# Kernel tuning notes

Hardware: AMD Instinct MI355X
Metric: run time of the kernel (lower is better)

## Reference

```python
import jax, jax.numpy as jnp
import numpy as np

B, S, D = 1, 2048, 1024
H = 16            # num_heads
DH = D // H       # head dim = 64
WIN = 128         # local window size
DIL = 4           # dilation rate


def setup_inputs() -> dict:
    key = jax.random.key(0)
    k1, k2, k3 = jax.random.split(key, 3)
    x = jax.random.normal(k1, (B, S, D), jnp.float32)
    w_qkv = jax.random.normal(k2, (D, 3 * D), jnp.float32) * 0.02
    w_out = jax.random.normal(k3, (D, D), jnp.float32) * 0.02
    return {"x": x, "w_qkv": w_qkv, "w_out": w_out}


def reference(x, w_qkv, w_out):
    b, s, d = x.shape
    scale = 1.0 / np.sqrt(DH).astype(np.float32)

    qkv = x @ w_qkv                                   # [B,S,3D]
    q, k, v = jnp.split(qkv, 3, axis=-1)
    q = q.reshape(b, s, H, DH)
    k = k.reshape(b, s, H, DH)
    v = v.reshape(b, s, H, DH)

    # ---- local window attention: attend within non-overlapping windows ----
    nw = s // WIN
    qw = q.reshape(b, nw, WIN, H, DH)
    kw = k.reshape(b, nw, WIN, H, DH)
    vw = v.reshape(b, nw, WIN, H, DH)
    s_loc = jnp.einsum('bnihd,bnjhd->bnhij', qw, kw) * scale
    p_loc = jax.nn.softmax(s_loc, axis=-1)
    o_loc = jnp.einsum('bnhij,bnjhd->bnihd', p_loc, vw).reshape(b, s, H, DH)

    # ---- dilated attention: attend within each stride-DIL residue class ----
    n = s // DIL
    # seq index = i*DIL + g  -> position i within dilation group g
    qd = q.reshape(b, n, DIL, H, DH)
    kd = k.reshape(b, n, DIL, H, DH)
    vd = v.reshape(b, n, DIL, H, DH)
    s_dil = jnp.einsum('bighd,bjghd->bghij', qd, kd) * scale
    p_dil = jax.nn.softmax(s_dil, axis=-1)
    o_dil = jnp.einsum('bghij,bjghd->bighd', p_dil, vd).reshape(b, s, H, DH)

    # ---- global full attention ----
    s_glb = jnp.einsum('bihd,bjhd->bhij', q, k) * scale
    p_glb = jax.nn.softmax(s_glb, axis=-1)
    o_glb = jnp.einsum('bhij,bjhd->bihd', p_glb, v)

    # fuse the three scales (uniform average) and project out
    o = (o_loc + o_dil + o_glb) * (1.0 / 3.0)
    return o.reshape(b, s, d) @ w_out
```

## Files before the change

kernel.cpp:

```cpp
#include <hip/hip_runtime.h>
#include <hip/hip_bf16.h>


typedef __attribute__((ext_vector_type(8))) short s8v;
typedef __attribute__((ext_vector_type(4))) float f4v;

#define QSCALE 0.18033688011112042f

__device__ __forceinline__ short f2bf(float f) {
  union { float f; unsigned u; } x; x.f = f;
  unsigned r = (x.u + 0x7FFF + ((x.u >> 16) & 1)) >> 16;
  return (short)r;
}
__device__ __forceinline__ f4v mfma16(s8v a, s8v b, f4v c) {
  return __builtin_amdgcn_mfma_f32_16x16x32_bf16(a, b, c, 0, 0, 0);
}
__device__ __forceinline__ void load_lds16(const void* g, void* l) {
  __builtin_amdgcn_global_load_lds(
      (const __attribute__((address_space(1))) unsigned int*)g,
      (__attribute__((address_space(3))) unsigned int*)l, 16, 0, 0);
}
__device__ __forceinline__ float exp2f_fast(float x) {
  return __builtin_amdgcn_exp2f(x);
}

__global__ __launch_bounds__(256)
void fill_const_kernel(float* __restrict__ out, int n, float v) {
  int i = blockIdx.x * 256 + threadIdx.x;
  if (i < n) out[i] = v;
}

__global__ __launch_bounds__(256)
void prep_fused(const float* __restrict__ wq, short* __restrict__ wqT,
                const float* __restrict__ wo, short* __restrict__ woT,
                const float* __restrict__ x, short* __restrict__ xb) {
  const int bx = blockIdx.x, t = threadIdx.x;
  __shared__ float T[64][69];
  if (bx >= 64) {
    if (x) {
      int cb = (bx - 64) * 16 + blockIdx.y;
      int i = (cb * 256 + t) * 4;
      float4 v = *reinterpret_cast<const float4*>(&x[i]);
      union { short s[4]; int2 p; } u;
      u.s[0] = f2bf(v.x); u.s[1] = f2bf(v.y); u.s[2] = f2bf(v.z); u.s[3] = f2bf(v.w);
      *reinterpret_cast<int2*>(&xb[i]) = u.p;
    }
    return;
  }
  const float* src; short* dst; int N, bxx;
  if (bx < 48) { src = wq; dst = wqT; N = 3072; bxx = bx; }
  else         { src = wo; dst = woT; N = 1024; bxx = bx - 48; }
  const int K = 1024;
  const int n0 = bxx * 64, k0 = blockIdx.y * 64;
  for (int jb = t; jb < 1024; jb += 256) {
    int r = jb >> 4, c4 = (jb & 15) * 4;
    float4 v = *reinterpret_cast<const float4*>(&src[(size_t)(k0 + r) * N + n0 + c4]);
    T[c4 + 0][r] = v.x; T[c4 + 1][r] = v.y; T[c4 + 2][r] = v.z; T[c4 + 3][r] = v.w;
  }
  __syncthreads();
  for (int jb = t; jb < 512; jb += 256) {
    int n = jb >> 3, k8 = (jb & 7) * 8;
    union { short s[8]; int4 v; } p;
#pragma unroll
    for (int i = 0; i < 8; ++i) p.s[i] = f2bf(T[n][k8 + i]);
    *reinterpret_cast<int4*>(&dst[(size_t)(n0 + n) * K + k0 + k8]) = p.v;
  }
}

__device__ __forceinline__ void g1_epilogue_store(
    int gcol, int grow0, const f4v& a,
    short* __restrict__ qb, short* __restrict__ kb, short* __restrict__ vT) {
  if (gcol >= 2048) {
    int d = gcol - 2048;
    int j = grow0 >> 2;
    int gb = ((j >> 6) << 6) + (((j >> 5) & 1) << 5) +
             (((j >> 2) & 3) << 3) + (((j >> 4) & 1) << 2) + (j & 3);
    size_t base = (size_t)d * 2048 + gb;
#pragma unroll
    for (int r = 0; r < 4; ++r)
      vT[base + (r << 9)] = f2bf(a[r]);
  } else {
    short* dst = (gcol < 1024) ? qb : kb;
    float sc = (gcol < 1024) ? QSCALE : 1.0f;
    int c = gcol & 1023;
#pragma unroll
    for (int r = 0; r < 4; ++r)
      dst[(size_t)(grow0 + r) * 1024 + c] = f2bf(a[r] * sc);
  }
}

template <int COUT, bool AF32, int NT>
__global__ __launch_bounds__(256)
void gemm_tile(const void* __restrict__ Av, const short* __restrict__ Bt,
               short* __restrict__ qb, short* __restrict__ kb,
               short* __restrict__ vT, float* __restrict__ co,
               int K, int N) {
  __shared__ __align__(16) short As[2][64 * 32];
  __shared__ __align__(16) short Bs[2][NT * 32];
  const int tid = threadIdx.x, wave = tid >> 6;
  const int li = tid & 63;
  const int row0 = blockIdx.y * 64, col0 = blockIdx.x * NT;
  const int lr = li & 15, quad = li >> 4, lk = quad * 8;
  constexpr int NTW = NT / 64;

  f4v acc[4][NTW];
#pragma unroll
  for (int i = 0; i < 4; ++i)
#pragma unroll
    for (int j = 0; j < NTW; ++j) acc[i][j] = (f4v){0.f, 0.f, 0.f, 0.f};

  for (int k0 = 0; k0 < K; k0 += 64) {
    __syncthreads();
#pragma unroll
    for (int kk = 0; kk < 2; ++kk) {
#pragma unroll
      for (int u = 0; u < NTW; ++u)
        load_lds16(Bt + (size_t)(col0 + u * 64 + (tid >> 2)) * K + k0 + kk * 32 + (tid & 3) * 8,
                   &Bs[kk][u * 2048 + wave * 512]);
      if (AF32) {
        const float* A = (const float*)Av;
#pragma unroll
        for (int c = 0; c < 2; ++c) {
          int j = c * 256 + tid;
          int r = j >> 3, c4 = (j & 7) * 4;
          float4 v = *reinterpret_cast<const float4*>(
              &A[(size_t)(row0 + r) * K + k0 + kk * 32 + c4]);
          union { short s[4]; int2 v2; } p;
          p.s[0] = f2bf(v.x); p.s[1] = f2bf(v.y); p.s[2] = f2bf(v.z); p.s[3] = f2bf(v.w);
          *reinterpret_cast<int2*>(&As[kk][r * 32 + c4]) = p.v2;
        }
      } else {
        load_lds16((const short*)Av + (size_t)(row0 + (tid >> 2)) * K + k0 + kk * 32 + (tid & 3) * 8,
                   &As[kk][wave * 512]);
      }
    }
    __syncthreads();

#pragma unroll
    for (int kk = 0; kk < 2; ++kk) {
      s8v af[4], bfr[NTW];
#pragma unroll
      for (int mt = 0; mt < 4; ++mt)
        af[mt] = *reinterpret_cast<const s8v*>(&As[kk][(mt * 16 + lr) * 32 + lk]);
#pragma unroll
      for (int u = 0; u < NTW; ++u)
        bfr[u] = *reinterpret_cast<const s8v*>(&Bs[kk][(wave * (NT / 4) + u * 16 + lr) * 32 + lk]);
#pragma unroll
      for (int mt = 0; mt < 4; ++mt)
#pragma unroll
        for (int u = 0; u < NTW; ++u)
          acc[mt][u] = mfma16(af[mt], bfr[u], acc[mt][u]);
    }
  }

#pragma unroll
  for (int mt = 0; mt < 4; ++mt) {
#pragma unroll
    for (int u = 0; u < NTW; ++u) {
      int gcol = col0 + wave * (NT / 4) + u * 16 + lr;
      int grow0 = row0 + mt * 16 + quad * 4;
      if (COUT == 0) {
        g1_epilogue_store(gcol, grow0, acc[mt][u], qb, kb, vT);
      } else {
#pragma unroll
        for (int r = 0; r < 4; ++r)
          co[(size_t)(grow0 + r) * N + gcol] = acc[mt][u][r] * (1.0f / 3.0f);
      }
    }
  }
}

__global__ __launch_bounds__(512, 2)
void attn_unified(const short* __restrict__ qb, const short* __restrict__ kb,
                  const short* __restrict__ vT, short* __restrict__ o) {
  __shared__ __align__(16) short Ks[2][64][72];
  __shared__ __align__(16) short Vt[2][64][72];
  __shared__ float lX[2][4][16][4];

  const int tid = threadIdx.x;
  const int wave = tid >> 6, li = tid & 63;
  const int grp = wave >> 2, wr = wave & 3;
  const int b = blockIdx.x, h = b & 15, g = b >> 4;
  const int qcol = h * 64;
  const int lr = li & 15, quad = li >> 4, lk = quad * 8;
  const int wt2 = g >> 2;
  const int wH  = (g >> 1) & 1;
  const bool wgrp = (grp == wH);
  const int sr = tid >> 3, sc8 = (tid & 7) * 8;

  s8v q0, q1;
  {
    const short* qrow = &qb[(size_t)(g * 64 + wr * 16 + lr) * 1024 + qcol];
    q0 = *reinterpret_cast<const s8v*>(&qrow[lk]);
    q1 = *reinterpret_cast<const s8v*>(&qrow[32 + lk]);
  }

  *reinterpret_cast<int4*>(&Ks[0][sr][sc8]) =
      *reinterpret_cast<const int4*>(&kb[(size_t)(sr << 2) * 1024 + qcol + sc8]);
  *reinterpret_cast<int4*>(&Vt[0][sr][sc8]) =
      *reinterpret_cast<const int4*>(&vT[(size_t)(h * 64 + sr) * 2048 + sc8]);
  __syncthreads();

  float l_r = 0.f, l_loc = 0.f, l_dil = 0.f;
  f4v oacc[4], o_loc[4], o_dil[4];
#pragma unroll
  for (int i = 0; i < 4; ++i) {
    oacc[i]  = (f4v){0.f, 0.f, 0.f, 0.f};
    o_loc[i] = (f4v){0.f, 0.f, 0.f, 0.f};
    o_dil[i] = (f4v){0.f, 0.f, 0.f, 0.f};
  }

  const int koffA = ((grp * 2 + 0) * 16 + lr) * 72 + lk;
  const int koffB = ((grp * 2 + 1) * 16 + lr) * 72 + lk;
  const short* KsF = &Ks[0][0][0];
  const short* VtF = &Vt[0][0][0];

#pragma unroll
  for (int rho = 0; rho < 4; ++rho) {
    const float sn0 = oacc[0][rho], sn1 = oacc[1][rho],
                sn2 = oacc[2][rho], sn3 = oacc[3][rho];
    const float lsn = l_r;

#pragma unroll 2
    for (int t8 = 0; t8 < 8; ++t8) {
      const int t = rho * 8 + t8;
      const int cur = t8 & 1, nxt = cur ^ 1;
      const bool pf = (rho < 3) || (t8 < 7);
      const bool wt = wgrp && (t8 == wt2);
      const int cb = cur * 4608;

      int4 kpre, vpre;
      if (pf) {
        const int tn = t + 1;
        const int ksn = ((((tn & 7) << 6) + sr) << 2) + (tn >> 3);
        kpre = *reinterpret_cast<const int4*>(&kb[(size_t)ksn * 1024 + qcol + sc8]);
        vpre = *reinterpret_cast<const int4*>(
            &vT[(size_t)(h * 64 + sr) * 2048 + tn * 64 + sc8]);
      }

      f4v s4a = (f4v){0.f, 0.f, 0.f, 0.f};
      f4v s4b = (f4v){0.f, 0.f, 0.f, 0.f};
      s4a = mfma16(*reinterpret_cast<const s8v*>(&KsF[cb + koffA]), q0, s4a);
      s4b = mfma16(*reinterpret_cast<const s8v*>(&KsF[cb + koffB]), q0, s4b);
      s4a = mfma16(*reinterpret_cast<const s8v*>(&KsF[cb + koffA + 32]), q1, s4a);
      s4b = mfma16(*reinterpret_cast<const s8v*>(&KsF[cb + koffB + 32]), q1, s4b);

      union { short s[8]; s8v v; } pk;
      float ps = 0.f;
#pragma unroll
      for (int r = 0; r < 4; ++r) {
        float p0 = exp2f_fast(s4a[r]), p1 = exp2f_fast(s4b[r]);
        ps += p0 + p1;
        pk.s[r] = f2bf(p0); pk.s[4 + r] = f2bf(p1);
      }
      l_r += ps;
      if (wt) l_loc += ps;

      if (wt) {
#pragma unroll
        for (int nt = 0; nt < 4; ++nt) {
          s8v bv = *reinterpret_cast<const s8v*>(
              &VtF[cb + (nt * 16 + lr) * 72 + grp * 32 + lk]);
          f4v dd = mfma16(pk.v, bv, (f4v){0.f, 0.f, 0.f, 0.f});
          oacc[nt] += dd;
          o_loc[nt] += dd;
        }
      } else {
#pragma unroll
        for (int nt = 0; nt < 4; ++nt) {
          s8v bv = *reinterpret_cast<const s8v*>(
              &VtF[cb + (nt * 16 + lr) * 72 + grp * 32 + lk]);
          oacc[nt] = mfma16(pk.v, bv, oacc[nt]);
        }
      }

      if (pf) {
        *reinterpret_cast<int4*>(&Ks[nxt][sr][sc8]) = kpre;
        *reinterpret_cast<int4*>(&Vt[nxt][sr][sc8]) = vpre;
      }
      __syncthreads();
    }

    if (((lr ^ rho) & 3) == 0) l_dil = l_r - lsn;
    o_dil[0][rho] = oacc[0][rho] - sn0;
    o_dil[1][rho] = oacc[1][rho] - sn1;
    o_dil[2][rho] = oacc[2][rho] - sn2;
    o_dil[3][rho] = oacc[3][rho] - sn3;
  }

  l_r   += __shfl_xor(l_r, 16);   l_r   += __shfl_xor(l_r, 32);
  l_loc += __shfl_xor(l_loc, 16); l_loc += __shfl_xor(l_loc, 32);
  l_dil += __shfl_xor(l_dil, 16); l_dil += __shfl_xor(l_dil, 32);
  if (li < 16) {
    lX[grp][wr][li][0] = l_r;
    lX[grp][wr][li][1] = l_loc;
    lX[grp][wr][li][2] = l_dil;
  }
  __syncthreads();

  f4v part[4];
#pragma unroll
  for (int r = 0; r < 4; ++r) {
    int q4 = quad * 4 + r;
    float lg = lX[0][wr][q4][0] + lX[1][wr][q4][0];
    float ll = lX[0][wr][q4][1] + lX[1][wr][q4][1];
    float ld = lX[0][wr][q4][2] + lX[1][wr][q4][2];
    float ig = 1.0f / lg, il = 1.0f / ll, id = 1.0f / ld;
#pragma unroll
    for (int nt = 0; nt < 4; ++nt)
      part[nt][r] = oacc[nt][r] * ig + o_loc[nt][r] * il + o_dil[nt][r] * id;
  }

  float* xch = reinterpret_cast<float*>(&Ks[0][0][0]);
  const int slot = wr * 64 + li;
  if (grp == 1) {
#pragma unroll
    for (int nt = 0; nt < 4; ++nt)
#pragma unroll
      for (int hh = 0; hh < 2; ++hh) {
        float2 v2 = make_float2(part[nt][2 * hh], part[nt][2 * hh + 1]);
        *reinterpret_cast<float2*>(&xch[slot * 18 + (nt * 2 + hh) * 2]) = v2;
      }
  }
  __syncthreads();
  if (grp == 0) {
#pragma unroll
    for (int nt = 0; nt < 4; ++nt)
#pragma unroll
      for (int hh = 0; hh < 2; ++hh) {
        float2 v2 = *reinterpret_cast<const float2*>(&xch[slot * 18 + (nt * 2 + hh) * 2]);
        part[nt][2 * hh]     += v2.x;
        part[nt][2 * hh + 1] += v2.y;
      }
#pragma unroll
    for (int r = 0; r < 4; ++r) {
      int qs = g * 64 + wr * 16 + quad * 4 + r;
#pragma unroll
      for (int nt = 0; nt < 4; ++nt)
        o[(size_t)qs * 1024 + qcol + nt * 16 + lr] = f2bf(part[nt][r]);
    }
  }
}

extern "C" void kernel_launch(void* const* d_in, const int* in_sizes, int n_in,
                              void* d_out, int out_size, void* d_ws, size_t ws_size,
                              hipStream_t stream) {
  float* out = (float*)d_out;
  const int nfill = (out_size + 255) / 256;
  if (n_in != 3) { fill_const_kernel<<<nfill, 256, 0, stream>>>(out, out_size, 0.5f); return; }
  int ix = -1, iq = -1, io = -1;
  for (int i = 0; i < 3; ++i) {
    if      (in_sizes[i] == 2097152) ix = i;
    else if (in_sizes[i] == 3145728) iq = i;
    else if (in_sizes[i] == 1048576) io = i;
  }
  if (ix < 0 || iq < 0 || io < 0) { fill_const_kernel<<<nfill, 256, 0, stream>>>(out, out_size, 0.3f); return; }
  const float* x     = (const float*)d_in[ix];
  const float* w_qkv = (const float*)d_in[iq];
  const float* w_out = (const float*)d_in[io];

  char* ws = (char*)d_ws;
  const size_t MB = 1048576;
  const size_t needX = 24 * MB;
  const size_t needY = 20 * MB;

  if (ws_size >= needX) {
    short* qb     = (short*)(ws);
    short* kb     = (short*)(ws + 4 * MB);
    short* vT     = (short*)(ws + 8 * MB);
    short* w_qkvT = (short*)(ws + 12 * MB);
    short* o      = (short*)(ws + 12 * MB);
    short* w_outT = (short*)(ws + 18 * MB);
    short* xb     = (short*)(ws + 20 * MB);
    prep_fused<<<dim3(192, 16), 256, 0, stream>>>(w_qkv, w_qkvT, w_out, w_outT, x, xb);
    gemm_tile<0, false, 128><<<dim3(24, 32), 256, 0, stream>>>(xb, w_qkvT, qb, kb, vT, nullptr, 1024, 3072);
    attn_unified<<<512, 512, 0, stream>>>(qb, kb, vT, o);
    gemm_tile<1, false, 64><<<dim3(16, 32), 256, 0, stream>>>(o, w_outT, nullptr, nullptr, nullptr, out, 1024, 1024);
  } else if (ws_size >= needY) {
    short* w_outT = (short*)(ws);
    short* qb     = (short*)(ws + 2 * MB);
    short* kb     = (short*)(ws + 6 * MB);
    short* vT     = (short*)(ws + 10 * MB);
    short* w_qkvT = (short*)(ws + 14 * MB);
    short* o      = (short*)(ws + 14 * MB);
    prep_fused<<<dim3(64, 16), 256, 0, stream>>>(w_qkv, w_qkvT, w_out, w_outT, nullptr, nullptr);
    gemm_tile<0, true, 128><<<dim3(24, 32), 256, 0, stream>>>(x, w_qkvT, qb, kb, vT, nullptr, 1024, 3072);
    attn_unified<<<512, 512, 0, stream>>>(qb, kb, vT, o);
    gemm_tile<1, false, 64><<<dim3(16, 32), 256, 0, stream>>>(o, w_outT, nullptr, nullptr, nullptr, out, 1024, 1024);
  } else {
    fill_const_kernel<<<nfill, 256, 0, stream>>>(out, out_size, 0.2f);
  }
}
```

Before: 149.8 us.

## Process two K/V tiles per barrier with four-slot LDS ring

The attention loop now handles two 64-key tiles per iteration using a 4-slot K/V shared-memory ring instead of a 2-slot double buffer, prefetching the next two tiles into registers. This halves the number of __syncthreads barriers and gives global loads more compute to hide behind. In exchange it doubles LDS use and register pressure for prefetched tiles, which may hurt occupancy at 2 blocks per CU.

```diff
diff --git a/kernel.cpp b/kernel.cpp
--- a/kernel.cpp
+++ b/kernel.cpp
@@ -173,8 +173,8 @@
 __global__ __launch_bounds__(512, 2)
 void attn_unified(const short* __restrict__ qb, const short* __restrict__ kb,
                   const short* __restrict__ vT, short* __restrict__ o) {
-  __shared__ __align__(16) short Ks[2][64][72];
-  __shared__ __align__(16) short Vt[2][64][72];
+  __shared__ __align__(16) short Ks[4][64][72];
+  __shared__ __align__(16) short Vt[4][64][72];
   __shared__ float lX[2][4][16][4];
 
   const int tid = threadIdx.x;
@@ -195,10 +195,14 @@
     q1 = *reinterpret_cast<const s8v*>(&qrow[32 + lk]);
   }
 
-  *reinterpret_cast<int4*>(&Ks[0][sr][sc8]) =
-      *reinterpret_cast<const int4*>(&kb[(size_t)(sr << 2) * 1024 + qcol + sc8]);
-  *reinterpret_cast<int4*>(&Vt[0][sr][sc8]) =
-      *reinterpret_cast<const int4*>(&vT[(size_t)(h * 64 + sr) * 2048 + sc8]);
+#pragma unroll
+  for (int c = 0; c < 2; ++c) {
+    int ks = (c * 64 + sr) << 2;
+    *reinterpret_cast<int4*>(&Ks[c][sr][sc8]) =
+        *reinterpret_cast<const int4*>(&kb[(size_t)ks * 1024 + qcol + sc8]);
+    *reinterpret_cast<int4*>(&Vt[c][sr][sc8]) =
+        *reinterpret_cast<const int4*>(&vT[(size_t)(h * 64 + sr) * 2048 + c * 64 + sc8]);
+  }
   __syncthreads();
 
   float l_r = 0.f, l_loc = 0.f, l_dil = 0.f;
@@ -212,6 +216,7 @@
 
   const int koffA = ((grp * 2 + 0) * 16 + lr) * 72 + lk;
   const int koffB = ((grp * 2 + 1) * 16 + lr) * 72 + lk;
+  const int voff  = lr * 72 + grp * 32 + lk;
   const short* KsF = &Ks[0][0][0];
   const short* VtF = &Vt[0][0][0];
 
@@ -222,61 +227,105 @@
     const float lsn = l_r;
 
 #pragma unroll 2
-    for (int t8 = 0; t8 < 8; ++t8) {
-      const int t = rho * 8 + t8;
-      const int cur = t8 & 1, nxt = cur ^ 1;
-      const bool pf = (rho < 3) || (t8 < 7);
-      const bool wt = wgrp && (t8 == wt2);
-      const int cb = cur * 4608;
-
-      int4 kpre, vpre;
+    for (int p8 = 0; p8 < 4; ++p8) {
+      const int tA = rho * 8 + 2 * p8;
+      const int bufA = (2 * p8) & 3;
+      const int cbA = bufA * 4608, cbB = cbA + 4608;
+      const bool pf = (tA < 30);
+      const bool wtA = wgrp && (2 * p8 == wt2);
+      const bool wtB = wgrp && (2 * p8 + 1 == wt2);
+
+      int4 kpA, vpA, kpB, vpB;
       if (pf) {
-        const int tn = t + 1;
-        const int ksn = ((((tn & 7) << 6) + sr) << 2) + (tn >> 3);
-        kpre = *reinterpret_cast<const int4*>(&kb[(size_t)ksn * 1024 + qcol + sc8]);
-        vpre = *reinterpret_cast<const int4*>(
-            &vT[(size_t)(h * 64 + sr) * 2048 + tn * 64 + sc8]);
-      }
-
-      f4v s4a = (f4v){0.f, 0.f, 0.f, 0.f};
-      f4v s4b = (f4v){0.f, 0.f, 0.f, 0.f};
-      s4a = mfma16(*reinterpret_cast<const s8v*>(&KsF[cb + koffA]), q0, s4a);
-      s4b = mfma16(*reinterpret_cast<const s8v*>(&KsF[cb + koffB]), q0, s4b);
-      s4a = mfma16(*reinterpret_cast<const s8v*>(&KsF[cb + koffA + 32]), q1, s4a);
-      s4b = mfma16(*reinterpret_cast<const s8v*>(&KsF[cb + koffB + 32]), q1, s4b);
-
-      union { short s[8]; s8v v; } pk;
-      float ps = 0.f;
-#pragma unroll
-      for (int r = 0; r < 4; ++r) {
-        float p0 = exp2f_fast(s4a[r]), p1 = exp2f_fast(s4b[r]);
-        ps += p0 + p1;
-        pk.s[r] = f2bf(p0); pk.s[4 + r] = f2bf(p1);
-      }
-      l_r += ps;
-      if (wt) l_loc += ps;
-
-      if (wt) {
-#pragma unroll
-        for (int nt = 0; nt < 4; ++nt) {
-          s8v bv = *reinterpret_cast<const s8v*>(
-              &VtF[cb + (nt * 16 + lr) * 72 + grp * 32 + lk]);
-          f4v dd = mfma16(pk.v, bv, (f4v){0.f, 0.f, 0.f, 0.f});
-          oacc[nt] += dd;
-          o_loc[nt] += dd;
+        const int tnA = tA + 2, tnB = tA + 3;
+        const int ksA = ((((tnA & 7) << 6) + sr) << 2) + (tnA >> 3);
+        const int ksB = ((((tnB & 7) << 6) + sr) << 2) + (tnB >> 3);
+        kpA = *reinterpret_cast<const int4*>(&kb[(size_t)ksA * 1024 + qcol + sc8]);
+        vpA = *reinterpret_cast<const int4*>(
+            &vT[(size_t)(h * 64 + sr) * 2048 + tnA * 64 + sc8]);
+        kpB = *reinterpret_cast<const int4*>(&kb[(size_t)ksB * 1024 + qcol + sc8]);
+        vpB = *reinterpret_cast<const int4*>(
+            &vT[(size_t)(h * 64 + sr) * 2048 + tnB * 64 + sc8]);
+      }
+
+      {
+        f4v s4a = (f4v){0.f, 0.f, 0.f, 0.f};
+        f4v s4b = (f4v){0.f, 0.f, 0.f, 0.f};
+        s4a = mfma16(*reinterpret_cast<const s8v*>(&KsF[cbA + koffA]), q0, s4a);
+        s4b = mfma16(*reinterpret_cast<const s8v*>(&KsF[cbA + koffB]), q0, s4b);
+        s4a = mfma16(*reinterpret_cast<const s8v*>(&KsF[cbA + koffA + 32]), q1, s4a);
+        s4b = mfma16(*reinterpret_cast<const s8v*>(&KsF[cbA + koffB + 32]), q1, s4b);
+
+        union { short s[8]; s8v v; } pk;
+        float ps = 0.f;
+#pragma unroll
+        for (int r = 0; r < 4; ++r) {
+          float p0 = exp2f_fast(s4a[r]), p1 = exp2f_fast(s4b[r]);
+          ps += p0 + p1;
+          pk.s[r] = f2bf(p0); pk.s[4 + r] = f2bf(p1);
         }
-      } else {
-#pragma unroll
-        for (int nt = 0; nt < 4; ++nt) {
-          s8v bv = *reinterpret_cast<const s8v*>(
-              &VtF[cb + (nt * 16 + lr) * 72 + grp * 32 + lk]);
-          oacc[nt] = mfma16(pk.v, bv, oacc[nt]);
+        l_r += ps;
+        if (wtA) l_loc += ps;
+
+        if (wtA) {
+#pragma unroll
+          for (int nt = 0; nt < 4; ++nt) {
+            s8v bv = *reinterpret_cast<const s8v*>(&VtF[cbA + nt * 1152 + voff]);
+            f4v dd = mfma16(pk.v, bv, (f4v){0.f, 0.f, 0.f, 0.f});
+            oacc[nt] += dd;
+            o_loc[nt] += dd;
+          }
+        } else {
+#pragma unroll
+          for (int nt = 0; nt < 4; ++nt) {
+            s8v bv = *reinterpret_cast<const s8v*>(&VtF[cbA + nt * 1152 + voff]);
+            oacc[nt] = mfma16(pk.v, bv, oacc[nt]);
+          }
         }
       }
 
+      {
+        f4v s4a = (f4v){0.f, 0.f, 0.f, 0.f};
+        f4v s4b = (f4v){0.f, 0.f, 0.f, 0.f};
+        s4a = mfma16(*reinterpret_cast<const s8v*>(&KsF[cbB + koffA]), q0, s4a);
+        s4b = mfma16(*reinterpret_cast<const s8v*>(&KsF[cbB + koffB]), q0, s4b);
+        s4a = mfma16(*reinterpret_cast<const s8v*>(&KsF[cbB + koffA + 32]), q1, s4a);
+        s4b = mfma16(*reinterpret_cast<const s8v*>(&KsF[cbB + koffB + 32]), q1, s4b);
+
+        union { short s[8]; s8v v; } pk;
+        float ps = 0.f;
+#pragma unroll
+        for (int r = 0; r < 4; ++r) {
+          float p0 = exp2f_fast(s4a[r]), p1 = exp2f_fast(s4b[r]);
+          ps += p0 + p1;
+          pk.s[r] = f2bf(p0); pk.s[4 + r] = f2bf(p1);
+        }
+        l_r += ps;
+        if (wtB) l_loc += ps;
+
+        if (wtB) {
+#pragma unroll
+          for (int nt = 0; nt < 4; ++nt) {
+            s8v bv = *reinterpret_cast<const s8v*>(&VtF[cbB + nt * 1152 + voff]);
+            f4v dd = mfma16(pk.v, bv, (f4v){0.f, 0.f, 0.f, 0.f});
+            oacc[nt] += dd;
+            o_loc[nt] += dd;
+          }
+        } else {
+#pragma unroll
+          for (int nt = 0; nt < 4; ++nt) {
+            s8v bv = *reinterpret_cast<const s8v*>(&VtF[cbB + nt * 1152 + voff]);
+            oacc[nt] = mfma16(pk.v, bv, oacc[nt]);
+          }
+        }
+      }
+
       if (pf) {
-        *reinterpret_cast<int4*>(&Ks[nxt][sr][sc8]) = kpre;
-        *reinterpret_cast<int4*>(&Vt[nxt][sr][sc8]) = vpre;
+        const int wbA = bufA ^ 2;
+        *reinterpret_cast<int4*>(&Ks[wbA][sr][sc8])     = kpA;
+        *reinterpret_cast<int4*>(&Vt[wbA][sr][sc8])     = vpA;
+        *reinterpret_cast<int4*>(&Ks[wbA + 1][sr][sc8]) = kpB;
+        *reinterpret_cast<int4*>(&Vt[wbA + 1][sr][sc8]) = vpB;
       }
       __syncthreads();
     }
```

After: 147.4 us. About the same (-1.6%).

## Load K/V fragments directly from global memory instead of LDS double buffering

Applied to the files above, without the earlier changes.

The attention kernel no longer stages K and V tiles through double-buffered shared memory with a block-wide barrier per step. Each wave now loads its MFMA operand fragments for K and transposed V straight from global memory, the step loop is fully unrolled, and blocks are remapped so that neighbouring block IDs cover different heads and groups. This removes 32 __syncthreads and the LDS round trip, but each wave now issues its own global loads, with redundant traffic across the four waves that share K/V and more reliance on L2 and cache hits.

```diff
diff --git a/kernel.cpp b/kernel.cpp
--- a/kernel.cpp
+++ b/kernel.cpp
@@ -173,20 +173,20 @@
 __global__ __launch_bounds__(512, 2)
 void attn_unified(const short* __restrict__ qb, const short* __restrict__ kb,
                   const short* __restrict__ vT, short* __restrict__ o) {
-  __shared__ __align__(16) short Ks[2][64][72];
-  __shared__ __align__(16) short Vt[2][64][72];
   __shared__ float lX[2][4][16][4];
+  __shared__ __align__(16) float xch[256 * 18];
 
   const int tid = threadIdx.x;
   const int wave = tid >> 6, li = tid & 63;
   const int grp = wave >> 2, wr = wave & 3;
-  const int b = blockIdx.x, h = b & 15, g = b >> 4;
+  const int b0 = blockIdx.x;
+  const int bs = (b0 & 7) * 64 + (b0 >> 3);
+  const int h = bs >> 5, g = bs & 31;
   const int qcol = h * 64;
   const int lr = li & 15, quad = li >> 4, lk = quad * 8;
   const int wt2 = g >> 2;
   const int wH  = (g >> 1) & 1;
   const bool wgrp = (grp == wH);
-  const int sr = tid >> 3, sc8 = (tid & 7) * 8;
 
   s8v q0, q1;
   {
@@ -195,11 +195,9 @@
     q1 = *reinterpret_cast<const s8v*>(&qrow[32 + lk]);
   }
 
-  *reinterpret_cast<int4*>(&Ks[0][sr][sc8]) =
-      *reinterpret_cast<const int4*>(&kb[(size_t)(sr << 2) * 1024 + qcol + sc8]);
-  *reinterpret_cast<int4*>(&Vt[0][sr][sc8]) =
-      *reinterpret_cast<const int4*>(&vT[(size_t)(h * 64 + sr) * 2048 + sc8]);
-  __syncthreads();
+  const int rowA = grp * 32 + lr;
+  const int rowB = rowA + 16;
+  const short* vrow = vT + ((size_t)(h * 64 + lr)) * 2048 + grp * 32 + lk;
 
   float l_r = 0.f, l_loc = 0.f, l_dil = 0.f;
   f4v oacc[4], o_loc[4], o_dil[4];
@@ -210,40 +208,35 @@
     o_dil[i] = (f4v){0.f, 0.f, 0.f, 0.f};
   }
 
-  const int koffA = ((grp * 2 + 0) * 16 + lr) * 72 + lk;
-  const int koffB = ((grp * 2 + 1) * 16 + lr) * 72 + lk;
-  const short* KsF = &Ks[0][0][0];
-  const short* VtF = &Vt[0][0][0];
-
 #pragma unroll
   for (int rho = 0; rho < 4; ++rho) {
     const float sn0 = oacc[0][rho], sn1 = oacc[1][rho],
                 sn2 = oacc[2][rho], sn3 = oacc[3][rho];
     const float lsn = l_r;
 
-#pragma unroll 2
+#pragma unroll
     for (int t8 = 0; t8 < 8; ++t8) {
       const int t = rho * 8 + t8;
-      const int cur = t8 & 1, nxt = cur ^ 1;
-      const bool pf = (rho < 3) || (t8 < 7);
       const bool wt = wgrp && (t8 == wt2);
-      const int cb = cur * 4608;
-
-      int4 kpre, vpre;
-      if (pf) {
-        const int tn = t + 1;
-        const int ksn = ((((tn & 7) << 6) + sr) << 2) + (tn >> 3);
-        kpre = *reinterpret_cast<const int4*>(&kb[(size_t)ksn * 1024 + qcol + sc8]);
-        vpre = *reinterpret_cast<const int4*>(
-            &vT[(size_t)(h * 64 + sr) * 2048 + tn * 64 + sc8]);
-      }
+
+      const size_t kra = ((size_t)(((t8 << 6) + rowA) << 2) + rho) * 1024 + qcol;
+      const size_t krb = ((size_t)(((t8 << 6) + rowB) << 2) + rho) * 1024 + qcol;
+      const s8v ka0 = *reinterpret_cast<const s8v*>(&kb[kra + lk]);
+      const s8v ka1 = *reinterpret_cast<const s8v*>(&kb[kra + 32 + lk]);
+      const s8v kb0 = *reinterpret_cast<const s8v*>(&kb[krb + lk]);
+      const s8v kb1 = *reinterpret_cast<const s8v*>(&kb[krb + 32 + lk]);
+      const short* vt0 = vrow + (size_t)t * 64;
+      const s8v v0 = *reinterpret_cast<const s8v*>(vt0);
+      const s8v v1 = *reinterpret_cast<const s8v*>(vt0 + 16 * 2048);
+      const s8v v2 = *reinterpret_cast<const s8v*>(vt0 + 32 * 2048);
+      const s8v v3 = *reinterpret_cast<const s8v*>(vt0 + 48 * 2048);
 
       f4v s4a = (f4v){0.f, 0.f, 0.f, 0.f};
       f4v s4b = (f4v){0.f, 0.f, 0.f, 0.f};
-      s4a = mfma16(*reinterpret_cast<const s8v*>(&KsF[cb + koffA]), q0, s4a);
-      s4b = mfma16(*reinterpret_cast<const s8v*>(&KsF[cb + koffB]), q0, s4b);
-      s4a = mfma16(*reinterpret_cast<const s8v*>(&KsF[cb + koffA + 32]), q1, s4a);
-      s4b = mfma16(*reinterpret_cast<const s8v*>(&KsF[cb + koffB + 32]), q1, s4b);
+      s4a = mfma16(ka0, q0, s4a);
+      s4b = mfma16(kb0, q0, s4b);
+      s4a = mfma16(ka1, q1, s4a);
+      s4b = mfma16(kb1, q1, s4b);
 
       union { short s[8]; s8v v; } pk;
       float ps = 0.f;
@@ -257,28 +250,20 @@
       if (wt) l_loc += ps;
 
       if (wt) {
-#pragma unroll
-        for (int nt = 0; nt < 4; ++nt) {
-          s8v bv = *reinterpret_cast<const s8v*>(
-              &VtF[cb + (nt * 16 + lr) * 72 + grp * 32 + lk]);
-          f4v dd = mfma16(pk.v, bv, (f4v){0.f, 0.f, 0.f, 0.f});
-          oacc[nt] += dd;
-          o_loc[nt] += dd;
-        }
+        f4v d0 = mfma16(pk.v, v0, (f4v){0.f, 0.f, 0.f, 0.f});
+        f4v d1 = mfma16(pk.v, v1, (f4v){0.f, 0.f, 0.f, 0.f});
+        f4v d2 = mfma16(pk.v, v2, (f4v){0.f, 0.f, 0.f, 0.f});
+        f4v d3 = mfma16(pk.v, v3, (f4v){0.f, 0.f, 0.f, 0.f});
+        oacc[0] += d0; o_loc[0] += d0;
+        oacc[1] += d1; o_loc[1] += d1;
+        oacc[2] += d2; o_loc[2] += d2;
+        oacc[3] += d3; o_loc[3] += d3;
       } else {
-#pragma unroll
-        for (int nt = 0; nt < 4; ++nt) {
-          s8v bv = *reinterpret_cast<const s8v*>(
-              &VtF[cb + (nt * 16 + lr) * 72 + grp * 32 + lk]);
-          oacc[nt] = mfma16(pk.v, bv, oacc[nt]);
-        }
-      }
-
-      if (pf) {
-        *reinterpret_cast<int4*>(&Ks[nxt][sr][sc8]) = kpre;
-        *reinterpret_cast<int4*>(&Vt[nxt][sr][sc8]) = vpre;
-      }
-      __syncthreads();
+        oacc[0] = mfma16(pk.v, v0, oacc[0]);
+        oacc[1] = mfma16(pk.v, v1, oacc[1]);
+        oacc[2] = mfma16(pk.v, v2, oacc[2]);
+        oacc[3] = mfma16(pk.v, v3, oacc[3]);
+      }
     }
 
     if (((lr ^ rho) & 3) == 0) l_dil = l_r - lsn;
@@ -311,7 +296,6 @@
       part[nt][r] = oacc[nt][r] * ig + o_loc[nt][r] * il + o_dil[nt][r] * id;
   }
 
-  float* xch = reinterpret_cast<float*>(&Ks[0][0][0]);
   const int slot = wr * 64 + li;
   if (grp == 1) {
 #pragma unroll
```

New measurement: 265.8 us. 77.4% more time.
